# Optimization experiments

Measured on AMD Instinct MI355X. Metric: run time of the kernel, lower is better.

## Reference

```python
import jax, jax.numpy as jnp
import numpy as np

B, C, W, H, HEADS = 8, 512, 32, 32, 8
DH = C // HEADS  # 64
N = W * H        # 1024


def setup_inputs() -> dict:
    key = jax.random.key(0)
    ks = jax.random.split(key, 10)
    s = 1.0 / np.sqrt(C)
    return {
        "x": jax.random.normal(ks[0], (B, C, W, H), jnp.float32),
        "d": jax.random.normal(ks[1], (B, C, W, H), jnp.float32),
        "Wq": jax.random.normal(ks[2], (C, C), jnp.float32) * s,
        "bq": jnp.zeros((C,), jnp.float32),
        "Wk": jax.random.normal(ks[3], (C, C), jnp.float32) * s,
        "bk": jnp.zeros((C,), jnp.float32),
        "Wv": jax.random.normal(ks[4], (C, C), jnp.float32) * s,
        "bv": jnp.zeros((C,), jnp.float32),
        "rel_h": jax.random.normal(ks[5], (1, HEADS, DH, 1, H), jnp.float32),
        "rel_w": jax.random.normal(ks[6], (1, HEADS, DH, W, 1), jnp.float32),
    }


def reference(x, d, Wq, bq, Wk, bk, Wv, bv, rel_h, rel_w):
    b, c, w, h = x.shape
    heads = rel_h.shape[1]
    dh = c // heads
    n = w * h

    def proj(t, Wt, bt):
        # 1x1 conv == per-pixel channel matmul; reshape to [B, heads, dh, N]
        y = jnp.einsum('bchw,oc->bohw', t, Wt) + bt[None, :, None, None]
        return y.reshape(b, heads, dh, n)

    q = proj(x, Wq, bq)
    k = proj(d, Wk, bk)
    v = proj(d, Wv, bv)

    # content-content: q^T k -> [B, h, N, N]
    cc = jnp.einsum('bhdn,bhdm->bhnm', q, k)
    # content-position: (rel_h + rel_w) broadcast -> [1, h, dh, N], then pos^T @ q
    pos = (rel_h + rel_w).reshape(heads, dh, n)
    cp = jnp.einsum('hdm,bhdn->bhmn', pos, q)

    attn = jax.nn.softmax(cc + cp, axis=-1)  # [B, h, N, N]
    # out = v @ attn^T : out[b,h,d,i] = sum_j v[b,h,d,j] * attn[b,h,i,j]
    out = jnp.einsum('bhdj,bhij->bhdi', v, attn)
    return out.reshape(b, c, w, h)
```

## Files before the change

### kernel.cpp

```cpp
#include <hip/hip_runtime.h>

typedef unsigned short u16;
typedef _Float16 f16x8 __attribute__((ext_vector_type(8)));
typedef float f32x4 __attribute__((ext_vector_type(4)));
typedef float f32x16 __attribute__((ext_vector_type(16)));

#define NB 8
#define NC 512
#define NHD 8
#define DH 64
#define NN 1024

__device__ __forceinline__ u16 f2h(float f) {
    union { _Float16 h; u16 u; } v; v.h = (_Float16)f;
    return v.u;
}

__global__ __launch_bounds__(256) void k_cvt(const float* __restrict__ a, const float* __restrict__ b,
                                             const float* __restrict__ c,
                                             u16* __restrict__ oa, u16* __restrict__ ob, u16* __restrict__ oc) {
    int i = blockIdx.x * 256 + threadIdx.x;
    const float* src = (blockIdx.y == 0) ? a : (blockIdx.y == 1) ? b : c;
    u16* dst = (blockIdx.y == 0) ? oa : (blockIdx.y == 1) ? ob : oc;
    dst[i] = f2h(src[i]);
}

__global__ __launch_bounds__(256) void k_pos(const float* __restrict__ relh, const float* __restrict__ relw,
                                             u16* __restrict__ ph) {
    int idx = blockIdx.x * 256 + threadIdx.x;
    int dd = idx & 63;
    int i  = (idx >> 6) & 1023;
    int h  = idx >> 16;
    float f = relh[(h * 64 + dd) * 32 + (i & 31)] + relw[(h * 64 + dd) * 32 + (i >> 5)];
    ph[(h * 1024 + i) * 64 + dd] = f2h(f);
}

__global__ __launch_bounds__(256) void k_t16(const float* __restrict__ x, const float* __restrict__ d,
                                             u16* __restrict__ xt, u16* __restrict__ dt) {
    __shared__ float tile[64][65];
    int nb = blockIdx.x * 64;
    int cb = blockIdx.y * 64;
    int b = blockIdx.z & 7;
    int which = blockIdx.z >> 3;
    const float* src = which ? d : x;
    u16* ot = which ? dt : xt;
    int t = threadIdx.x;
    {
        int crow = t >> 2, n0 = (t & 3) * 16;
        const float* g = src + ((size_t)(b * NC + cb + crow)) * NN + nb + n0;
#pragma unroll
        for (int k = 0; k < 16; k += 4) {
            float4 v = *(const float4*)(g + k);
            tile[crow][n0 + k + 0] = v.x;
            tile[crow][n0 + k + 1] = v.y;
            tile[crow][n0 + k + 2] = v.z;
            tile[crow][n0 + k + 3] = v.w;
        }
    }
    __syncthreads();
    {
        int nrow = t >> 2, c0 = (t & 3) * 16;
        union { u16 s[16]; uint4 v[2]; } uh;
#pragma unroll
        for (int k = 0; k < 16; ++k) uh.s[k] = f2h(tile[c0 + k][nrow]);
        size_t oidx = ((size_t)(b * NN + nb + nrow)) * NC + cb + c0;
        *(uint4*)(ot + oidx)     = uh.v[0];
        *(uint4*)(ot + oidx + 8) = uh.v[1];
    }
}

__global__ __launch_bounds__(256) void k_proj(
    const u16* __restrict__ xt, const u16* __restrict__ dt,
    const u16* __restrict__ wq, const u16* __restrict__ wk, const u16* __restrict__ wv,
    const float* __restrict__ bq, const float* __restrict__ bk, const float* __restrict__ bv,
    u16* __restrict__ qt_o, u16* __restrict__ kt_o, u16* __restrict__ v_o) {
    __shared__ u16 Asm[128 * 32];
    __shared__ u16 Bsm[128 * 32];

    int p = blockIdx.z % 3;
    int b = blockIdx.z / 3;
    const u16 *Ap, *Bp;
    const float* bias;
    u16* Oq;
    if (p == 0)      { Ap = wq; Bp = xt; bias = bq; Oq = qt_o; }
    else if (p == 1) { Ap = wk; Bp = dt; bias = bk; Oq = kt_o; }
    else             { Ap = wv; Bp = dt; bias = bv; Oq = v_o; }
    Bp += (size_t)b * NN * NC;

    int obase = blockIdx.x * 128;
    int nbase = blockIdx.y * 128;
    int t = threadIdx.x, wave = t >> 6, quad = (t & 63) >> 4, l15 = t & 15;
    int wr = (wave >> 1) * 64, wc = (wave & 1) * 64;

    f32x4 acc[4][4];
#pragma unroll
    for (int fo = 0; fo < 4; ++fo)
#pragma unroll
        for (int fn = 0; fn < 4; ++fn)
#pragma unroll
            for (int r = 0; r < 4; ++r) acc[fo][fn][r] = 0.f;

    for (int kk = 0; kk < NC; kk += 32) {
        __syncthreads();
#pragma unroll
        for (int u = 0; u < 2; ++u) {
            int c = u * 256 + t;
            int row = c >> 2, part = c & 3;
            __builtin_amdgcn_global_load_lds(
                (const __attribute__((address_space(1))) void*)(Ap + (size_t)(obase + row) * NC + kk + part * 8),
                (__attribute__((address_space(3))) void*)(Asm + (size_t)(u * 256 + wave * 64) * 8), 16, 0, 0);
            __builtin_amdgcn_global_load_lds(
                (const __attribute__((address_space(1))) void*)(Bp + (size_t)(nbase + row) * NC + kk + part * 8),
                (__attribute__((address_space(3))) void*)(Bsm + (size_t)(u * 256 + wave * 64) * 8), 16, 0, 0);
        }
        __syncthreads();

        f16x8 af[4], bfr[4];
#pragma unroll
        for (int fo = 0; fo < 4; ++fo) af[fo] = *(const f16x8*)&Asm[(wr + fo * 16 + l15) * 32 + quad * 8];
#pragma unroll
        for (int fn = 0; fn < 4; ++fn) bfr[fn] = *(const f16x8*)&Bsm[(wc + fn * 16 + l15) * 32 + quad * 8];
#pragma unroll
        for (int fo = 0; fo < 4; ++fo)
#pragma unroll
            for (int fn = 0; fn < 4; ++fn)
                acc[fo][fn] = __builtin_amdgcn_mfma_f32_16x16x32_f16(af[fo], bfr[fn], acc[fo][fn], 0, 0, 0);
    }

#pragma unroll
    for (int fo = 0; fo < 4; ++fo) {
#pragma unroll
        for (int fn = 0; fn < 4; ++fn) {
            int o0 = obase + wr + fo * 16 + quad * 4;
            int n = nbase + wc + fn * 16 + l15;
            if (p < 2) {
                union { u16 s[4]; uint2 v2; } uh;
#pragma unroll
                for (int r = 0; r < 4; ++r) uh.s[r] = f2h(acc[fo][fn][r] + bias[o0 + r]);
                int head = o0 >> 6, dd0 = o0 & 63;
                size_t idx = (((size_t)(b * NHD + head) * NN) + n) * DH + dd0;
                *(uint2*)&Oq[idx] = uh.v2;
            } else {
#pragma unroll
                for (int r = 0; r < 4; ++r) {
                    int o = o0 + r;
                    int head = o >> 6, dd = o & 63;
                    Oq[((size_t)(b * NHD + head) * DH + dd) * NN + n] = f2h(acc[fo][fn][r] + bias[o]);
                }
            }
        }
    }
}

__global__ __launch_bounds__(256) void k_attn(
    const u16* __restrict__ qt, const u16* __restrict__ kt,
    const u16* __restrict__ v_, const u16* __restrict__ pos,
    float* __restrict__ out) {
    __shared__ u16 Bs[64 * 136];
    __shared__ u16 Vt[64 * 72];
    __shared__ u16 Pt[128 * 72];

    int ib = blockIdx.x, head = blockIdx.y, b = blockIdx.z;
    int t = threadIdx.x, ws = t >> 6, lane = t & 63, h = lane >> 5, l31 = lane & 31;
    size_t bh = (size_t)(b * NHD + head);
    const u16* qb = qt + bh * NN * DH;
    const u16* kb = kt + bh * NN * DH;
    const u16* vb = v_ + bh * DH * NN;
    const u16* pb = pos + (size_t)head * NN * DH;
    int i0 = ib * 128;
    int iglob = i0 + ws * 32 + l31;

    f16x8 qf[8];
#pragma unroll
    for (int ks = 0; ks < 4; ++ks) qf[ks] = *(const f16x8*)&qb[(size_t)iglob * DH + ks * 16 + h * 8];
#pragma unroll
    for (int ks = 4; ks < 8; ++ks) qf[ks] = *(const f16x8*)&pb[(size_t)iglob * DH + (ks - 4) * 16 + h * 8];

    f32x16 oacc[2];
#pragma unroll
    for (int df = 0; df < 2; ++df)
#pragma unroll
        for (int r = 0; r < 16; ++r) oacc[df][r] = 0.f;
    float m_ = -__builtin_inff(), l_ = 0.f;
    int ptb = ws * 32 * 72;

    for (int jc = 0; jc < NN; jc += 64) {
        __syncthreads();
#pragma unroll
        for (int u = 0; u < 4; ++u) {
            int c = u * 256 + t;
            int row = c >> 4, g = c & 15;
            const u16* src = (g < 8) ? &kb[(size_t)(jc + row) * DH + g * 8]
                                     : &qb[(size_t)(jc + row) * DH + (g - 8) * 8];
            *(uint4*)&Bs[row * 136 + g * 8] = *(const uint4*)src;
        }
#pragma unroll
        for (int u = 0; u < 2; ++u) {
            int c = u * 256 + t;
            int row = c >> 3, g = c & 7;
            *(uint4*)&Vt[row * 72 + g * 8] = *(const uint4*)&vb[(size_t)row * NN + jc + g * 8];
        }
        __syncthreads();

        f32x16 sacc[2];
#pragma unroll
        for (int jf = 0; jf < 2; ++jf)
#pragma unroll
            for (int r = 0; r < 16; ++r) sacc[jf][r] = 0.f;
#pragma unroll
        for (int jf = 0; jf < 2; ++jf)
#pragma unroll
            for (int ks = 0; ks < 8; ++ks) {
                f16x8 af = *(const f16x8*)&Bs[(jf * 32 + l31) * 136 + ks * 16 + h * 8];
                sacc[jf] = __builtin_amdgcn_mfma_f32_32x32x16_f16(af, qf[ks], sacc[jf], 0, 0, 0);
            }

        float mloc = -__builtin_inff();
#pragma unroll
        for (int jf = 0; jf < 2; ++jf)
#pragma unroll
            for (int r = 0; r < 16; ++r) mloc = fmaxf(mloc, sacc[jf][r]);
        mloc = fmaxf(mloc, __shfl_xor(mloc, 32));
        float mnew = fmaxf(m_, mloc);
        float alpha = __expf(m_ - mnew);
        m_ = mnew;
        float lsum = 0.f;
#pragma unroll
        for (int jf = 0; jf < 2; ++jf)
#pragma unroll
            for (int r = 0; r < 16; ++r) {
                float pv = __expf(sacc[jf][r] - mnew);
                sacc[jf][r] = pv;
                lsum += pv;
            }
        lsum += __shfl_xor(lsum, 32);
        l_ = l_ * alpha + lsum;

#pragma unroll
        for (int jf = 0; jf < 2; ++jf)
#pragma unroll
            for (int mm = 0; mm < 4; ++mm) {
                union { _Float16 q[4]; uint2 u2; } w;
#pragma unroll
                for (int r = 0; r < 4; ++r) w.q[r] = (_Float16)sacc[jf][mm * 4 + r];
                *(uint2*)&Pt[ptb + l31 * 72 + jf * 32 + 4 * h + 8 * mm] = w.u2;
            }

#pragma unroll
        for (int df = 0; df < 2; ++df)
#pragma unroll
            for (int r = 0; r < 16; ++r) oacc[df][r] *= alpha;
#pragma unroll
        for (int jw = 0; jw < 4; ++jw) {
            f16x8 pf = *(const f16x8*)&Pt[ptb + l31 * 72 + jw * 16 + h * 8];
#pragma unroll
            for (int df = 0; df < 2; ++df) {
                f16x8 vf = *(const f16x8*)&Vt[(df * 32 + l31) * 72 + jw * 16 + h * 8];
                oacc[df] = __builtin_amdgcn_mfma_f32_32x32x16_f16(vf, pf, oacc[df], 0, 0, 0);
            }
        }
    }

    float li = 1.0f / l_;
#pragma unroll
    for (int df = 0; df < 2; ++df)
#pragma unroll
        for (int r = 0; r < 16; ++r) {
            int d = df * 32 + (r & 3) + 8 * (r >> 2) + 4 * h;
            out[((size_t)(b * NC) + head * DH + d) * NN + i0 + ws * 32 + l31] = oacc[df][r] * li;
        }
}

#define SXT  (8u * 1024u * 512u * 2u)
#define SW   (512u * 512u * 2u)
#define SQT  SXT
#define SPOS (8u * 1024u * 64u * 2u)

#define OFF_XT   (0u)
#define OFF_DT   (OFF_XT + SXT)
#define OFF_WQ   (OFF_DT + SXT)
#define OFF_WK   (OFF_WQ + SW)
#define OFF_WV   (OFF_WK + SW)
#define OFF_QT   (OFF_WV + SW)
#define OFF_KT   (OFF_QT + SQT)
#define OFF_V    (OFF_KT + SQT)
#define OFF_POS  (OFF_V + SQT)

extern "C" void kernel_launch(void* const* d_in, const int* in_sizes, int n_in,
                              void* d_out, int out_size, void* d_ws, size_t ws_size,
                              hipStream_t stream) {
    const float* x   = (const float*)d_in[0];
    const float* d   = (const float*)d_in[1];
    const float* Wq  = (const float*)d_in[2];
    const float* bq  = (const float*)d_in[3];
    const float* Wk  = (const float*)d_in[4];
    const float* bk  = (const float*)d_in[5];
    const float* Wv  = (const float*)d_in[6];
    const float* bv  = (const float*)d_in[7];
    const float* rh  = (const float*)d_in[8];
    const float* rw  = (const float*)d_in[9];

    char* ws = (char*)d_ws;
    u16* xt = (u16*)(ws + OFF_XT);
    u16* dt = (u16*)(ws + OFF_DT);
    u16* wq = (u16*)(ws + OFF_WQ);
    u16* wk = (u16*)(ws + OFF_WK);
    u16* wv = (u16*)(ws + OFF_WV);
    u16* qt = (u16*)(ws + OFF_QT);
    u16* kt = (u16*)(ws + OFF_KT);
    u16* v_ = (u16*)(ws + OFF_V);
    u16* ps = (u16*)(ws + OFF_POS);

    k_cvt<<<dim3(1024, 3), 256, 0, stream>>>(Wq, Wk, Wv, wq, wk, wv);
    k_pos<<<2048, 256, 0, stream>>>(rh, rw, ps);
    k_t16<<<dim3(16, 8, 16), 256, 0, stream>>>(x, d, xt, dt);
    k_proj<<<dim3(4, 8, 24), 256, 0, stream>>>(xt, dt, wq, wk, wv, bq, bk, bv, qt, kt, v_);
    k_attn<<<dim3(8, 8, 8), 256, 0, stream>>>(qt, kt, v_, ps, (float*)d_out);
}
```

Baseline: 177.1 us.

## Merge prep kernels, widen attention key tiles, use exp2 softmax with lazy rescale

The three preprocessing kernels (weight conversion, position table, transpose) are merged into one launch. Q is pre-scaled by log2(e) in the projection so the softmax can use native exp2, and the running-max rescale of the accumulators is skipped when no lane's max grows. The attention loop now processes 128 keys per iteration, with new LDS padding, packed fp16 conversion and a flattened block index, which means fewer barriers and loop trips. The cost is more LDS and registers per block, which may limit occupancy despite the launch_bounds hint.

```diff
diff --git a/kernel.cpp b/kernel.cpp
--- a/kernel.cpp
+++ b/kernel.cpp
@@ -2,6 +2,7 @@
 
 typedef unsigned short u16;
 typedef _Float16 f16x8 __attribute__((ext_vector_type(8)));
+typedef __fp16 hf16x2 __attribute__((ext_vector_type(2)));
 typedef float f32x4 __attribute__((ext_vector_type(4)));
 typedef float f32x16 __attribute__((ext_vector_type(16)));
 
@@ -10,62 +11,65 @@
 #define NHD 8
 #define DH 64
 #define NN 1024
+#define LOG2E 1.4426950408889634f
 
 __device__ __forceinline__ u16 f2h(float f) {
     union { _Float16 h; u16 u; } v; v.h = (_Float16)f;
     return v.u;
 }
 
-__global__ __launch_bounds__(256) void k_cvt(const float* __restrict__ a, const float* __restrict__ b,
-                                             const float* __restrict__ c,
-                                             u16* __restrict__ oa, u16* __restrict__ ob, u16* __restrict__ oc) {
-    int i = blockIdx.x * 256 + threadIdx.x;
-    const float* src = (blockIdx.y == 0) ? a : (blockIdx.y == 1) ? b : c;
-    u16* dst = (blockIdx.y == 0) ? oa : (blockIdx.y == 1) ? ob : oc;
-    dst[i] = f2h(src[i]);
-}
-
-__global__ __launch_bounds__(256) void k_pos(const float* __restrict__ relh, const float* __restrict__ relw,
-                                             u16* __restrict__ ph) {
-    int idx = blockIdx.x * 256 + threadIdx.x;
-    int dd = idx & 63;
-    int i  = (idx >> 6) & 1023;
-    int h  = idx >> 16;
-    float f = relh[(h * 64 + dd) * 32 + (i & 31)] + relw[(h * 64 + dd) * 32 + (i >> 5)];
-    ph[(h * 1024 + i) * 64 + dd] = f2h(f);
-}
-
-__global__ __launch_bounds__(256) void k_t16(const float* __restrict__ x, const float* __restrict__ d,
-                                             u16* __restrict__ xt, u16* __restrict__ dt) {
+__global__ __launch_bounds__(256) void k_prep(
+    const float* __restrict__ x, const float* __restrict__ d,
+    const float* __restrict__ Wq, const float* __restrict__ Wk, const float* __restrict__ Wv,
+    const float* __restrict__ relh, const float* __restrict__ relw,
+    u16* __restrict__ xt, u16* __restrict__ dt,
+    u16* __restrict__ wq, u16* __restrict__ wk, u16* __restrict__ wv,
+    u16* __restrict__ ps) {
     __shared__ float tile[64][65];
-    int nb = blockIdx.x * 64;
-    int cb = blockIdx.y * 64;
-    int b = blockIdx.z & 7;
-    int which = blockIdx.z >> 3;
-    const float* src = which ? d : x;
-    u16* ot = which ? dt : xt;
-    int t = threadIdx.x;
-    {
-        int crow = t >> 2, n0 = (t & 3) * 16;
-        const float* g = src + ((size_t)(b * NC + cb + crow)) * NN + nb + n0;
-#pragma unroll
-        for (int k = 0; k < 16; k += 4) {
-            float4 v = *(const float4*)(g + k);
-            tile[crow][n0 + k + 0] = v.x;
-            tile[crow][n0 + k + 1] = v.y;
-            tile[crow][n0 + k + 2] = v.z;
-            tile[crow][n0 + k + 3] = v.w;
-        }
-    }
-    __syncthreads();
-    {
-        int nrow = t >> 2, c0 = (t & 3) * 16;
-        union { u16 s[16]; uint4 v[2]; } uh;
-#pragma unroll
-        for (int k = 0; k < 16; ++k) uh.s[k] = f2h(tile[c0 + k][nrow]);
-        size_t oidx = ((size_t)(b * NN + nb + nrow)) * NC + cb + c0;
-        *(uint4*)(ot + oidx)     = uh.v[0];
-        *(uint4*)(ot + oidx + 8) = uh.v[1];
+    int id = blockIdx.x, t = threadIdx.x;
+    if (id < 2048) {
+        int nb = (id & 15) * 64;
+        int cb = ((id >> 4) & 7) * 64;
+        int z = id >> 7;
+        int b = z & 7;
+        const float* src = (z >> 3) ? d : x;
+        u16* ot = (z >> 3) ? dt : xt;
+        {
+            int crow = t >> 2, n0 = (t & 3) * 16;
+            const float* g = src + ((size_t)(b * NC + cb + crow)) * NN + nb + n0;
+#pragma unroll
+            for (int k = 0; k < 16; k += 4) {
+                float4 v = *(const float4*)(g + k);
+                tile[crow][n0 + k + 0] = v.x;
+                tile[crow][n0 + k + 1] = v.y;
+                tile[crow][n0 + k + 2] = v.z;
+                tile[crow][n0 + k + 3] = v.w;
+            }
+        }
+        __syncthreads();
+        {
+            int nrow = t >> 2, c0 = (t & 3) * 16;
+            union { u16 s[16]; uint4 v[2]; } uh;
+#pragma unroll
+            for (int k = 0; k < 16; ++k) uh.s[k] = f2h(tile[c0 + k][nrow]);
+            size_t oidx = ((size_t)(b * NN + nb + nrow)) * NC + cb + c0;
+            *(uint4*)(ot + oidx)     = uh.v[0];
+            *(uint4*)(ot + oidx + 8) = uh.v[1];
+        }
+    } else if (id < 5120) {
+        int j = id - 2048;
+        int m = j >> 10;
+        int i = (j & 1023) * 256 + t;
+        const float* src = (m == 0) ? Wq : (m == 1) ? Wk : Wv;
+        u16* dst = (m == 0) ? wq : (m == 1) ? wk : wv;
+        dst[i] = f2h(src[i]);
+    } else {
+        int idx = (id - 5120) * 256 + t;
+        int dd = idx & 63;
+        int i  = (idx >> 6) & 1023;
+        int h  = idx >> 16;
+        float f = relh[(h * 64 + dd) * 32 + (i & 31)] + relw[(h * 64 + dd) * 32 + (i >> 5)];
+        ps[(h * 1024 + i) * 64 + dd] = f2h(f);
     }
 }
 
@@ -86,6 +90,7 @@
     else if (p == 1) { Ap = wk; Bp = dt; bias = bk; Oq = kt_o; }
     else             { Ap = wv; Bp = dt; bias = bv; Oq = v_o; }
     Bp += (size_t)b * NN * NC;
+    float oscale = (p == 0) ? LOG2E : 1.0f;
 
     int obase = blockIdx.x * 128;
     int nbase = blockIdx.y * 128;
@@ -136,7 +141,7 @@
             if (p < 2) {
                 union { u16 s[4]; uint2 v2; } uh;
 #pragma unroll
-                for (int r = 0; r < 4; ++r) uh.s[r] = f2h(acc[fo][fn][r] + bias[o0 + r]);
+                for (int r = 0; r < 4; ++r) uh.s[r] = f2h((acc[fo][fn][r] + bias[o0 + r]) * oscale);
                 int head = o0 >> 6, dd0 = o0 & 63;
                 size_t idx = (((size_t)(b * NHD + head) * NN) + n) * DH + dd0;
                 *(uint2*)&Oq[idx] = uh.v2;
@@ -152,15 +157,19 @@
     }
 }
 
-__global__ __launch_bounds__(256) void k_attn(
+__global__ __launch_bounds__(256, 2) void k_attn(
     const u16* __restrict__ qt, const u16* __restrict__ kt,
     const u16* __restrict__ v_, const u16* __restrict__ pos,
     float* __restrict__ out) {
-    __shared__ u16 Bs[64 * 136];
-    __shared__ u16 Vt[64 * 72];
-    __shared__ u16 Pt[128 * 72];
-
-    int ib = blockIdx.x, head = blockIdx.y, b = blockIdx.z;
+    __shared__ u16 Bs[128 * 132];
+    __shared__ u16 Vt[64 * 132];
+    __shared__ u16 Pt[4 * 32 * 68];
+
+    int n = blockIdx.x;
+    int g = n & 63;
+    int ib = n >> 6;
+    int head = g & 7, b = g >> 3;
+
     int t = threadIdx.x, ws = t >> 6, lane = t & 63, h = lane >> 5, l31 = lane & 31;
     size_t bh = (size_t)(b * NHD + head);
     const u16* qb = qt + bh * NN * DH;
@@ -182,81 +191,89 @@
 #pragma unroll
         for (int r = 0; r < 16; ++r) oacc[df][r] = 0.f;
     float m_ = -__builtin_inff(), l_ = 0.f;
-    int ptb = ws * 32 * 72;
-
-    for (int jc = 0; jc < NN; jc += 64) {
-        __syncthreads();
+    int ptb = ws * 32 * 68;
+
+    for (int jc = 0; jc < NN; jc += 128) {
+        __syncthreads();
+#pragma unroll
+        for (int u = 0; u < 8; ++u) {
+            int c = u * 256 + t;
+            int row = c >> 4, gg = c & 15;
+            const u16* src = (gg < 8) ? &kb[(size_t)(jc + row) * DH + gg * 8]
+                                      : &qb[(size_t)(jc + row) * DH + (gg - 8) * 8];
+            *(uint4*)&Bs[row * 132 + gg * 8] = *(const uint4*)src;
+        }
 #pragma unroll
         for (int u = 0; u < 4; ++u) {
             int c = u * 256 + t;
-            int row = c >> 4, g = c & 15;
-            const u16* src = (g < 8) ? &kb[(size_t)(jc + row) * DH + g * 8]
-                                     : &qb[(size_t)(jc + row) * DH + (g - 8) * 8];
-            *(uint4*)&Bs[row * 136 + g * 8] = *(const uint4*)src;
-        }
-#pragma unroll
-        for (int u = 0; u < 2; ++u) {
-            int c = u * 256 + t;
-            int row = c >> 3, g = c & 7;
-            *(uint4*)&Vt[row * 72 + g * 8] = *(const uint4*)&vb[(size_t)row * NN + jc + g * 8];
-        }
-        __syncthreads();
-
-        f32x16 sacc[2];
-#pragma unroll
-        for (int jf = 0; jf < 2; ++jf)
+            int row = c >> 4, gg = c & 15;
+            *(uint4*)&Vt[row * 132 + gg * 8] = *(const uint4*)&vb[(size_t)row * NN + jc + gg * 8];
+        }
+        __syncthreads();
+
+        f32x16 sacc[4];
+#pragma unroll
+        for (int jf = 0; jf < 4; ++jf)
 #pragma unroll
             for (int r = 0; r < 16; ++r) sacc[jf][r] = 0.f;
 #pragma unroll
-        for (int jf = 0; jf < 2; ++jf)
+        for (int jf = 0; jf < 4; ++jf)
 #pragma unroll
             for (int ks = 0; ks < 8; ++ks) {
-                f16x8 af = *(const f16x8*)&Bs[(jf * 32 + l31) * 136 + ks * 16 + h * 8];
+                f16x8 af = *(const f16x8*)&Bs[(jf * 32 + l31) * 132 + ks * 16 + h * 8];
                 sacc[jf] = __builtin_amdgcn_mfma_f32_32x32x16_f16(af, qf[ks], sacc[jf], 0, 0, 0);
             }
 
         float mloc = -__builtin_inff();
 #pragma unroll
-        for (int jf = 0; jf < 2; ++jf)
+        for (int jf = 0; jf < 4; ++jf)
 #pragma unroll
             for (int r = 0; r < 16; ++r) mloc = fmaxf(mloc, sacc[jf][r]);
         mloc = fmaxf(mloc, __shfl_xor(mloc, 32));
-        float mnew = fmaxf(m_, mloc);
-        float alpha = __expf(m_ - mnew);
-        m_ = mnew;
+        if (__any(mloc > m_)) {
+            float mnew = fmaxf(m_, mloc);
+            float alpha = __builtin_amdgcn_exp2f(m_ - mnew);
+            m_ = mnew;
+#pragma unroll
+            for (int df = 0; df < 2; ++df)
+#pragma unroll
+                for (int r = 0; r < 16; ++r) oacc[df][r] *= alpha;
+            l_ *= alpha;
+        }
         float lsum = 0.f;
 #pragma unroll
-        for (int jf = 0; jf < 2; ++jf)
+        for (int jf = 0; jf < 4; ++jf)
 #pragma unroll
             for (int r = 0; r < 16; ++r) {
-                float pv = __expf(sacc[jf][r] - mnew);
+                float pv = __builtin_amdgcn_exp2f(sacc[jf][r] - m_);
                 sacc[jf][r] = pv;
                 lsum += pv;
             }
         lsum += __shfl_xor(lsum, 32);
-        l_ = l_ * alpha + lsum;
-
-#pragma unroll
-        for (int jf = 0; jf < 2; ++jf)
-#pragma unroll
-            for (int mm = 0; mm < 4; ++mm) {
-                union { _Float16 q[4]; uint2 u2; } w;
-#pragma unroll
-                for (int r = 0; r < 4; ++r) w.q[r] = (_Float16)sacc[jf][mm * 4 + r];
-                *(uint2*)&Pt[ptb + l31 * 72 + jf * 32 + 4 * h + 8 * mm] = w.u2;
-            }
-
-#pragma unroll
-        for (int df = 0; df < 2; ++df)
-#pragma unroll
-            for (int r = 0; r < 16; ++r) oacc[df][r] *= alpha;
-#pragma unroll
-        for (int jw = 0; jw < 4; ++jw) {
-            f16x8 pf = *(const f16x8*)&Pt[ptb + l31 * 72 + jw * 16 + h * 8];
-#pragma unroll
-            for (int df = 0; df < 2; ++df) {
-                f16x8 vf = *(const f16x8*)&Vt[(df * 32 + l31) * 72 + jw * 16 + h * 8];
-                oacc[df] = __builtin_amdgcn_mfma_f32_32x32x16_f16(vf, pf, oacc[df], 0, 0, 0);
+        l_ += lsum;
+
+#pragma unroll
+        for (int half = 0; half < 2; ++half) {
+#pragma unroll
+            for (int jf = 0; jf < 2; ++jf) {
+                int jfg = half * 2 + jf;
+#pragma unroll
+                for (int mm = 0; mm < 4; ++mm) {
+                    union { hf16x2 v; unsigned u; } p0, p1;
+                    p0.v = __builtin_amdgcn_cvt_pkrtz(sacc[jfg][mm * 4 + 0], sacc[jfg][mm * 4 + 1]);
+                    p1.v = __builtin_amdgcn_cvt_pkrtz(sacc[jfg][mm * 4 + 2], sacc[jfg][mm * 4 + 3]);
+                    uint2 w; w.x = p0.u; w.y = p1.u;
+                    *(uint2*)&Pt[ptb + l31 * 68 + jf * 32 + 4 * h + 8 * mm] = w;
+                }
+            }
+#pragma unroll
+            for (int jw = 0; jw < 4; ++jw) {
+                f16x8 pf = *(const f16x8*)&Pt[ptb + l31 * 68 + jw * 16 + h * 8];
+#pragma unroll
+                for (int df = 0; df < 2; ++df) {
+                    f16x8 vf = *(const f16x8*)&Vt[(df * 32 + l31) * 132 + half * 64 + jw * 16 + h * 8];
+                    oacc[df] = __builtin_amdgcn_mfma_f32_32x32x16_f16(vf, pf, oacc[df], 0, 0, 0);
+                }
             }
         }
     }
@@ -266,8 +283,8 @@
     for (int df = 0; df < 2; ++df)
 #pragma unroll
         for (int r = 0; r < 16; ++r) {
-            int d = df * 32 + (r & 3) + 8 * (r >> 2) + 4 * h;
-            out[((size_t)(b * NC) + head * DH + d) * NN + i0 + ws * 32 + l31] = oacc[df][r] * li;
+            int dd = df * 32 + (r & 3) + 8 * (r >> 2) + 4 * h;
+            out[((size_t)(b * NC) + head * DH + dd) * NN + i0 + ws * 32 + l31] = oacc[df][r] * li;
         }
 }
 
@@ -311,9 +328,7 @@
     u16* v_ = (u16*)(ws + OFF_V);
     u16* ps = (u16*)(ws + OFF_POS);
 
-    k_cvt<<<dim3(1024, 3), 256, 0, stream>>>(Wq, Wk, Wv, wq, wk, wv);
-    k_pos<<<2048, 256, 0, stream>>>(rh, rw, ps);
-    k_t16<<<dim3(16, 8, 16), 256, 0, stream>>>(x, d, xt, dt);
+    k_prep<<<7168, 256, 0, stream>>>(x, d, Wq, Wk, Wv, rh, rw, xt, dt, wq, wk, wv, ps);
     k_proj<<<dim3(4, 8, 24), 256, 0, stream>>>(xt, dt, wq, wk, wv, bq, bk, bv, qt, kt, v_);
-    k_attn<<<dim3(8, 8, 8), 256, 0, stream>>>(qt, kt, v_, ps, (float*)d_out);
-}
+    k_attn<<<512, 256, 0, stream>>>(qt, kt, v_, ps, (float*)d_out);
+}
```

Measured after the change: 167.0 us, median of 2. -5.7%, faster.
